# Performance work log

Hardware: AMD Instinct MI355X
Metric: run time of the kernel (lower is better)

## Reference

```python
import jax, jax.numpy as jnp
import numpy as np

LN_EPS = 1e-5
BITS = 4
MAX_VAL = (1 << (BITS - 1)) - 1  # 7 for 4-bit


def fwht(x):
    """Unnormalized fast Walsh-Hadamard transform along the last axis.
    Equivalent to the recursive torch hadamard_transform (H_n = H2 (x) H_{n/2})."""
    orig_shape = x.shape
    n = orig_shape[-1]
    x = x.reshape(-1, n)
    h = 1
    while h < n:
        x = x.reshape(-1, n // (2 * h), 2, h)
        a, b = x[:, :, 0, :], x[:, :, 1, :]
        x = jnp.stack([a + b, a - b], axis=2)
        x = x.reshape(-1, n)
        h *= 2
    return x.reshape(orig_shape)


def layer_norm(x, gamma, beta):
    mu = jnp.mean(x, axis=-1, keepdims=True)
    var = jnp.mean(jnp.square(x - mu), axis=-1, keepdims=True)
    return (x - mu) * jax.lax.rsqrt(var + LN_EPS) * gamma + beta


def activation_quantize(x):
    scale = jnp.clip(jnp.max(jnp.abs(x), axis=-1, keepdims=True), 1e-6, 1e6)
    sf = jnp.clip(MAX_VAL / scale, 1e-6, 1e6)
    return jnp.clip(jnp.round(x * sf), -MAX_VAL, MAX_VAL)


def weight_quantize(w):
    scale = jnp.mean(jnp.abs(w))
    wq = jnp.where(w > 0.5 * scale, 1.0, jnp.where(w < -0.5 * scale, -1.0, 0.0))
    return wq, scale


def setup_inputs() -> dict:
    key = jax.random.key(0)
    k1, k2 = jax.random.split(key)
    B, S, D_IN, D_OUT = 4, 2048, 4096, 4096
    x = jax.random.normal(k1, (B, S, D_IN), dtype=jnp.float32)
    gamma = jnp.ones((D_IN,), dtype=jnp.float32)
    beta = jnp.zeros((D_IN,), dtype=jnp.float32)
    # kaiming_uniform with a=sqrt(5): bound = sqrt(6/((1+5)*fan_in)) = 1/sqrt(fan_in)
    bound = 1.0 / np.sqrt(D_IN)
    weight = jax.random.uniform(k2, (D_OUT, D_IN), dtype=jnp.float32,
                                minval=-bound, maxval=bound)
    return {"x": x, "gamma": gamma, "beta": beta, "weight": weight}


def reference(x, gamma, beta, weight):
    x_ln = layer_norm(x, gamma, beta)            # [B,S,D]
    x_q = activation_quantize(x_ln)              # 4-bit values in [-7,7]
    x_h = fwht(x_q)                              # Hadamard of quantized acts
    w_q, w_scale = weight_quantize(weight)       # ternary * scalar scale
    out = jnp.einsum('bsd,od->bso', x_h, w_q * w_scale)
    out = fwht(out)                              # Hadamard on outputs
    return out
```

## Files before the change

kernel.cpp:

```cpp
#include <hip/hip_runtime.h>
#include <stdint.h>

typedef int i32x4 __attribute__((ext_vector_type(4)));

#define PIDX(e) ((e) + ((e) >> 5))

__device__ __forceinline__ float wred_sum(float v) {
#pragma unroll
    for (int o = 32; o > 0; o >>= 1) v += __shfl_down(v, o, 64);
    return v;
}
__device__ __forceinline__ float wred_max(float v) {
#pragma unroll
    for (int o = 32; o > 0; o >>= 1) v = fmaxf(v, __shfl_down(v, o, 64));
    return v;
}
__device__ __forceinline__ float bred_sum(float v, float* sb, int tid) {
    v = wred_sum(v);
    __syncthreads();
    if ((tid & 63) == 0) sb[tid >> 6] = v;
    __syncthreads();
    return sb[0] + sb[1] + sb[2] + sb[3];
}
__device__ __forceinline__ float bred_max(float v, float* sb, int tid) {
    v = wred_max(v);
    __syncthreads();
    if ((tid & 63) == 0) sb[tid >> 6] = v;
    __syncthreads();
    return fmaxf(fmaxf(sb[0], sb[1]), fmaxf(sb[2], sb[3]));
}

__device__ __forceinline__ int pack4(int a, int b, int c, int d) {
    return (a & 0xff) | ((b & 0xff) << 8) | ((c & 0xff) << 16) | ((d & 0xff) << 24);
}

__device__ __forceinline__ void fwht16(float v[16]) {
#pragma unroll
    for (int h = 1; h < 16; h <<= 1) {
#pragma unroll
        for (int i = 0; i < 16; ++i) {
            if ((i & h) == 0) {
                float a = v[i], b = v[i + h];
                v[i] = a + b;
                v[i + h] = a - b;
            }
        }
    }
}

__device__ void fwht4096(float* f, int t) {
    __syncthreads();
    float v[16];
    {
        int base = t << 4;
#pragma unroll
        for (int i = 0; i < 16; ++i) v[i] = f[PIDX(base + i)];
        fwht16(v);
#pragma unroll
        for (int i = 0; i < 16; ++i) f[PIDX(base + i)] = v[i];
    }
    __syncthreads();
    {
        int base = ((t >> 4) << 8) | (t & 15);
#pragma unroll
        for (int i = 0; i < 16; ++i) v[i] = f[PIDX(base + (i << 4))];
        fwht16(v);
#pragma unroll
        for (int i = 0; i < 16; ++i) f[PIDX(base + (i << 4))] = v[i];
    }
    __syncthreads();
    {
        int base = t;
#pragma unroll
        for (int i = 0; i < 16; ++i) v[i] = f[PIDX(base + (i << 8))];
        fwht16(v);
#pragma unroll
        for (int i = 0; i < 16; ++i) f[PIDX(base + (i << 8))] = v[i];
    }
    __syncthreads();
}

__global__ __launch_bounds__(256) void k_wabs(const float* __restrict__ w,
                                              float* __restrict__ partials) {
    __shared__ float sb[4];
    const int t = threadIdx.x;
    const int b = blockIdx.x;
    float acc = 0.0f;
#pragma unroll
    for (int i = 0; i < 8; ++i) {
        float4 f = *(const float4*)(w + (size_t)(b * 2048 + i * 256 + t) * 4);
        acc += fabsf(f.x) + fabsf(f.y) + fabsf(f.z) + fabsf(f.w);
    }
    float tot = bred_sum(acc, sb, t);
    if (t == 0) partials[b] = tot;
}

__global__ __launch_bounds__(256) void k_wscale(const float* __restrict__ partials,
                                                float* __restrict__ sfinal) {
    __shared__ float sb[4];
    const int t = threadIdx.x;
    float a = 0.0f;
#pragma unroll
    for (int i = 0; i < 8; ++i) a += partials[t + i * 256];
    float tot = bred_sum(a, sb, t);
    if (t == 0) sfinal[0] = tot * (1.0f / 16777216.0f);
}

__global__ __launch_bounds__(256) void k_wprep(const float* __restrict__ w,
                                               const float* __restrict__ sfinal,
                                               int8_t* __restrict__ hi,
                                               int8_t* __restrict__ lo) {
    __shared__ float f[4224];
    const int t = threadIdx.x;
    const int o = blockIdx.x;
    const float thr = 0.5f * sfinal[0];
    const float* wr = w + (size_t)o * 4096;
#pragma unroll
    for (int j = 0; j < 4; ++j) {
        float4 g = *(const float4*)(wr + j * 1024 + t * 4);
        int e = j * 1024 + t * 4;
        f[PIDX(e + 0)] = (g.x > thr) ? 1.0f : ((g.x < -thr) ? -1.0f : 0.0f);
        f[PIDX(e + 1)] = (g.y > thr) ? 1.0f : ((g.y < -thr) ? -1.0f : 0.0f);
        f[PIDX(e + 2)] = (g.z > thr) ? 1.0f : ((g.z < -thr) ? -1.0f : 0.0f);
        f[PIDX(e + 3)] = (g.w > thr) ? 1.0f : ((g.w < -thr) ? -1.0f : 0.0f);
    }
    fwht4096(f, t);
    int* hi32 = (int*)hi;
    int* lo32 = (int*)lo;
#pragma unroll
    for (int j = 0; j < 4; ++j) {
        int e = j * 1024 + t * 4;
        int l4[4], h4[4];
#pragma unroll
        for (int q = 0; q < 4; ++q) {
            int v = __float2int_rn(f[PIDX(e + q)]);
            int lv = ((v + 128) & 255) - 128;
            int hv = (v - lv) >> 8;
            l4[q] = lv; h4[q] = hv;
        }
        lo32[(size_t)o * 1024 + j * 256 + t] = pack4(l4[0], l4[1], l4[2], l4[3]);
        hi32[(size_t)o * 1024 + j * 256 + t] = pack4(h4[0], h4[1], h4[2], h4[3]);
    }
}

__global__ __launch_bounds__(256) void k_lnq(const float* __restrict__ x,
                                             const float* __restrict__ gamma,
                                             const float* __restrict__ beta,
                                             int8_t* __restrict__ xq) {
    __shared__ float sb[4];
    const int t = threadIdx.x;
    const size_t row = blockIdx.x;
    const float* xr = x + row * 4096;
    float v[16];
#pragma unroll
    for (int j = 0; j < 4; ++j) {
        float4 g = *(const float4*)(xr + j * 1024 + t * 4);
        v[j * 4 + 0] = g.x; v[j * 4 + 1] = g.y; v[j * 4 + 2] = g.z; v[j * 4 + 3] = g.w;
    }
    float s = 0.0f;
#pragma unroll
    for (int i = 0; i < 16; ++i) s += v[i];
    const float mu = bred_sum(s, sb, t) * (1.0f / 4096.0f);
    float sq = 0.0f;
#pragma unroll
    for (int i = 0; i < 16; ++i) { float d = v[i] - mu; sq += d * d; }
    const float var = bred_sum(sq, sb, t) * (1.0f / 4096.0f);
    const float rstd = rsqrtf(var + 1e-5f);
#pragma unroll
    for (int j = 0; j < 4; ++j) {
        float4 g = *(const float4*)(gamma + j * 1024 + t * 4);
        float4 b = *(const float4*)(beta + j * 1024 + t * 4);
        v[j * 4 + 0] = (v[j * 4 + 0] - mu) * rstd * g.x + b.x;
        v[j * 4 + 1] = (v[j * 4 + 1] - mu) * rstd * g.y + b.y;
        v[j * 4 + 2] = (v[j * 4 + 2] - mu) * rstd * g.z + b.z;
        v[j * 4 + 3] = (v[j * 4 + 3] - mu) * rstd * g.w + b.w;
    }
    float am = 0.0f;
#pragma unroll
    for (int i = 0; i < 16; ++i) am = fmaxf(am, fabsf(v[i]));
    am = bred_max(am, sb, t);
    const float scale = fminf(fmaxf(am, 1e-6f), 1e6f);
    const float sf = fminf(fmaxf(7.0f / scale, 1e-6f), 1e6f);
    int* xq32 = (int*)xq;
#pragma unroll
    for (int j = 0; j < 4; ++j) {
        int q4[4];
#pragma unroll
        for (int q = 0; q < 4; ++q) {
            float qq = rintf(v[j * 4 + q] * sf);
            qq = fminf(fmaxf(qq, -7.0f), 7.0f);
            q4[q] = (int)qq;
        }
        xq32[row * 1024 + j * 256 + t] = pack4(q4[0], q4[1], q4[2], q4[3]);
    }
}

__device__ __forceinline__ void gl_lds16(const void* g, void* l) {
    __builtin_amdgcn_global_load_lds(
        (const __attribute__((address_space(1))) void*)g,
        (__attribute__((address_space(3))) void*)l, 16, 0, 0);
}

__global__ __launch_bounds__(256, 2) void k_gemm(const int8_t* __restrict__ xq,
                                                 const int8_t* __restrict__ hi,
                                                 const int8_t* __restrict__ lo,
                                                 const float* __restrict__ sfinal,
                                                 float* __restrict__ out) {
    __shared__ __align__(16) int8_t sA[128 * 64];
    __shared__ __align__(16) int8_t sH[128 * 64];
    __shared__ __align__(16) int8_t sL[128 * 64];
    const int tid = threadIdx.x;
    const int lane = tid & 63, wid = tid >> 6;
    const int wr = wid >> 1, wc = wid & 1;
    const int bid = blockIdx.x;
    const int wg = (bid & 7) * 256 + (bid >> 3);
    const int bm = wg & 63, bn = wg >> 6;
    const int row0 = bm * 128, col0 = bn * 128;

    const int srow = lane >> 2;
    const int csw = ((lane & 3) ^ ((srow >> 1) & 3)) * 16;
    const int8_t* gA = xq + (size_t)(row0 + wid * 32 + srow) * 4096 + csw;
    const int8_t* gH = hi + (size_t)(col0 + wid * 32 + srow) * 4096 + csw;
    const int8_t* gL = lo + (size_t)(col0 + wid * 32 + srow) * 4096 + csw;
    int8_t* lA = sA + wid * 2048 + lane * 16;
    int8_t* lH = sH + wid * 2048 + lane * 16;
    int8_t* lL = sL + wid * 2048 + lane * 16;

    const int frow = lane & 15;
    const int pr = ((lane >> 4) ^ ((frow >> 1) & 3)) * 16;
    const int aoff = (wr * 64 + frow) * 64 + pr;
    const int boff = (wc * 64 + frow) * 64 + pr;

    i32x4 accL[4][4] = {};
    i32x4 accH[4][4] = {};

    for (int kt = 0; kt < 4096; kt += 64) {
        gl_lds16(gA + kt, lA);
        gl_lds16(gA + kt + 16 * 4096, lA + 1024);
        gl_lds16(gH + kt, lH);
        gl_lds16(gH + kt + 16 * 4096, lH + 1024);
        gl_lds16(gL + kt, lL);
        gl_lds16(gL + kt + 16 * 4096, lL + 1024);
        __syncthreads();

        i32x4 a[4], bh[4], bl[4];
#pragma unroll
        for (int m = 0; m < 4; ++m) a[m] = *(const i32x4*)(sA + aoff + m * 1024);
#pragma unroll
        for (int n = 0; n < 4; ++n) {
            bh[n] = *(const i32x4*)(sH + boff + n * 1024);
            bl[n] = *(const i32x4*)(sL + boff + n * 1024);
        }
#pragma unroll
        for (int m = 0; m < 4; ++m)
#pragma unroll
            for (int n = 0; n < 4; ++n) {
                accL[m][n] = __builtin_amdgcn_mfma_i32_16x16x64_i8(a[m], bl[n], accL[m][n], 0, 0, 0);
                accH[m][n] = __builtin_amdgcn_mfma_i32_16x16x64_i8(a[m], bh[n], accH[m][n], 0, 0, 0);
            }
        __syncthreads();
    }

    const float s = sfinal[0];
    const int orow0 = row0 + wr * 64 + (lane >> 4) * 4;
    const int ocol0 = col0 + wc * 64 + frow;
#pragma unroll
    for (int m = 0; m < 4; ++m)
#pragma unroll
        for (int n = 0; n < 4; ++n)
#pragma unroll
            for (int r = 0; r < 4; ++r) {
                int val = accL[m][n][r] + (accH[m][n][r] << 8);
                out[(size_t)(orow0 + m * 16 + r) * 4096 + (ocol0 + n * 16)] = s * (float)val;
            }
}

__global__ __launch_bounds__(256) void k_fwht_out(float* __restrict__ out) {
    __shared__ float f[4224];
    const int t = threadIdx.x;
    float* row = out + (size_t)blockIdx.x * 4096;
#pragma unroll
    for (int j = 0; j < 4; ++j) {
        float4 g = *(const float4*)(row + j * 1024 + t * 4);
        int e = j * 1024 + t * 4;
        f[PIDX(e + 0)] = g.x; f[PIDX(e + 1)] = g.y;
        f[PIDX(e + 2)] = g.z; f[PIDX(e + 3)] = g.w;
    }
    fwht4096(f, t);
#pragma unroll
    for (int j = 0; j < 4; ++j) {
        int e = j * 1024 + t * 4;
        float4 g;
        g.x = f[PIDX(e + 0)]; g.y = f[PIDX(e + 1)];
        g.z = f[PIDX(e + 2)]; g.w = f[PIDX(e + 3)];
        *(float4*)(row + e) = g;
    }
}

extern "C" void kernel_launch(void* const* d_in, const int* in_sizes, int n_in,
                              void* d_out, int out_size, void* d_ws, size_t ws_size,
                              hipStream_t stream) {
    const float* x     = (const float*)d_in[0];
    const float* gamma = (const float*)d_in[1];
    const float* beta  = (const float*)d_in[2];
    const float* w     = (const float*)d_in[3];
    float* out = (float*)d_out;

    char* ws = (char*)d_ws;
    float* sfinal   = (float*)ws;
    float* partials = (float*)(ws + 256);
    int8_t* xq  = (int8_t*)(ws + 16384);
    int8_t* whi = (int8_t*)(ws + 16384 + 33554432);
    int8_t* wlo = (int8_t*)(ws + 16384 + 33554432 + 16777216);

    k_wabs  <<<2048, 256, 0, stream>>>(w, partials);
    k_wscale<<<   1, 256, 0, stream>>>(partials, sfinal);
    k_wprep <<<4096, 256, 0, stream>>>(w, sfinal, whi, wlo);
    k_lnq   <<<8192, 256, 0, stream>>>(x, gamma, beta, xq);
    k_gemm  <<<2048, 256, 0, stream>>>(xq, whi, wlo, sfinal, out);
    k_fwht_out<<<8192, 256, 0, stream>>>(out);
}
```

Before: 620.6 us.

## Double-buffer int8 GEMM with 256x128 tiles, 8 waves and split MFMA phases

Result: slower. 725.5 us (+16.9%).

```diff
diff --git a/kernel.cpp b/kernel.cpp
--- a/kernel.cpp
+++ b/kernel.cpp
@@ -201,69 +201,120 @@
         (__attribute__((address_space(3))) void*)l, 16, 0, 0);
 }
 
-__global__ __launch_bounds__(256, 2) void k_gemm(const int8_t* __restrict__ xq,
+__global__ __launch_bounds__(512, 2) void k_gemm(const int8_t* __restrict__ xq,
                                                  const int8_t* __restrict__ hi,
                                                  const int8_t* __restrict__ lo,
                                                  const float* __restrict__ sfinal,
                                                  float* __restrict__ out) {
-    __shared__ __align__(16) int8_t sA[128 * 64];
-    __shared__ __align__(16) int8_t sH[128 * 64];
-    __shared__ __align__(16) int8_t sL[128 * 64];
+    __shared__ __align__(16) int8_t sA[2][16384];
+    __shared__ __align__(16) int8_t sH[2][8192];
+    __shared__ __align__(16) int8_t sL[2][8192];
     const int tid = threadIdx.x;
     const int lane = tid & 63, wid = tid >> 6;
-    const int wr = wid >> 1, wc = wid & 1;
+    const int wm = wid >> 1, wn = wid & 1;
     const int bid = blockIdx.x;
-    const int wg = (bid & 7) * 256 + (bid >> 3);
-    const int bm = wg & 63, bn = wg >> 6;
-    const int row0 = bm * 128, col0 = bn * 128;
-
-    const int srow = lane >> 2;
-    const int csw = ((lane & 3) ^ ((srow >> 1) & 3)) * 16;
-    const int8_t* gA = xq + (size_t)(row0 + wid * 32 + srow) * 4096 + csw;
-    const int8_t* gH = hi + (size_t)(col0 + wid * 32 + srow) * 4096 + csw;
-    const int8_t* gL = lo + (size_t)(col0 + wid * 32 + srow) * 4096 + csw;
-    int8_t* lA = sA + wid * 2048 + lane * 16;
-    int8_t* lH = sH + wid * 2048 + lane * 16;
-    int8_t* lL = sL + wid * 2048 + lane * 16;
+    const int wg = (bid & 7) * 128 + (bid >> 3);
+    const int bm = wg & 31, bn = wg >> 5;
+    const int row0 = bm * 256, col0 = bn * 128;
+
+    const int srow = tid >> 2;
+    const int scol = (((tid & 3) ^ ((srow >> 1) & 3))) * 16;
+    const int8_t* gA0 = xq + (size_t)(row0 + srow) * 4096 + scol;
+    const int8_t* gA1 = gA0 + (size_t)128 * 4096;
+    const int8_t* gH0 = hi + (size_t)(col0 + srow) * 4096 + scol;
+    const int8_t* gL0 = lo + (size_t)(col0 + srow) * 4096 + scol;
+    int8_t* dA = (int8_t*)sA + tid * 16;
+    int8_t* dH = (int8_t*)sH + tid * 16;
+    int8_t* dL = (int8_t*)sL + tid * 16;
+
+#define STAGE(buf_, kt_) do { const int o_ = (kt_) * 64;            \
+        gl_lds16(gA0 + o_, dA + (buf_) * 16384);                    \
+        gl_lds16(gA1 + o_, dA + (buf_) * 16384 + 8192);             \
+        gl_lds16(gH0 + o_, dH + (buf_) * 8192);                     \
+        gl_lds16(gL0 + o_, dL + (buf_) * 8192); } while (0)
 
     const int frow = lane & 15;
-    const int pr = ((lane >> 4) ^ ((frow >> 1) & 3)) * 16;
-    const int aoff = (wr * 64 + frow) * 64 + pr;
-    const int boff = (wc * 64 + frow) * 64 + pr;
+    const int kg = lane >> 4;
+    const int swz = ((kg ^ ((frow >> 1) & 3))) * 16;
+    const int aoff = (wm * 64 + frow) * 64 + swz;
+    const int boff = (wn * 64 + frow) * 64 + swz;
 
     i32x4 accL[4][4] = {};
     i32x4 accH[4][4] = {};
 
-    for (int kt = 0; kt < 4096; kt += 64) {
-        gl_lds16(gA + kt, lA);
-        gl_lds16(gA + kt + 16 * 4096, lA + 1024);
-        gl_lds16(gH + kt, lH);
-        gl_lds16(gH + kt + 16 * 4096, lH + 1024);
-        gl_lds16(gL + kt, lL);
-        gl_lds16(gL + kt + 16 * 4096, lL + 1024);
-        __syncthreads();
-
-        i32x4 a[4], bh[4], bl[4];
-#pragma unroll
-        for (int m = 0; m < 4; ++m) a[m] = *(const i32x4*)(sA + aoff + m * 1024);
-#pragma unroll
-        for (int n = 0; n < 4; ++n) {
-            bh[n] = *(const i32x4*)(sH + boff + n * 1024);
-            bl[n] = *(const i32x4*)(sL + boff + n * 1024);
-        }
-#pragma unroll
-        for (int m = 0; m < 4; ++m)
-#pragma unroll
-            for (int n = 0; n < 4; ++n) {
-                accL[m][n] = __builtin_amdgcn_mfma_i32_16x16x64_i8(a[m], bl[n], accL[m][n], 0, 0, 0);
-                accH[m][n] = __builtin_amdgcn_mfma_i32_16x16x64_i8(a[m], bh[n], accH[m][n], 0, 0, 0);
-            }
-        __syncthreads();
-    }
+    STAGE(0, 0);
+    asm volatile("s_waitcnt vmcnt(0)" ::: "memory");
+    asm volatile("s_barrier" ::: "memory");
+
+    for (int kt = 0; kt < 64; ++kt) {
+        const int cur = kt & 1;
+        const int8_t* A = sA[cur];
+        const int8_t* H = sH[cur];
+        const int8_t* L = sL[cur];
+
+        if (kt < 63) STAGE(cur ^ 1, kt + 1);
+        i32x4 a0 = *(const i32x4*)(A + aoff);
+        i32x4 a1 = *(const i32x4*)(A + aoff + 1024);
+        i32x4 a2 = *(const i32x4*)(A + aoff + 2048);
+        i32x4 a3 = *(const i32x4*)(A + aoff + 3072);
+        i32x4 h0 = *(const i32x4*)(H + boff);
+        i32x4 h1 = *(const i32x4*)(H + boff + 1024);
+        i32x4 l0 = *(const i32x4*)(L + boff);
+        i32x4 l1 = *(const i32x4*)(L + boff + 1024);
+        asm volatile("s_barrier" ::: "memory");
+        asm volatile("s_waitcnt lgkmcnt(0)" ::: "memory");
+        __builtin_amdgcn_s_setprio(1);
+        accL[0][0] = __builtin_amdgcn_mfma_i32_16x16x64_i8(a0, l0, accL[0][0], 0, 0, 0);
+        accH[0][0] = __builtin_amdgcn_mfma_i32_16x16x64_i8(a0, h0, accH[0][0], 0, 0, 0);
+        accL[0][1] = __builtin_amdgcn_mfma_i32_16x16x64_i8(a0, l1, accL[0][1], 0, 0, 0);
+        accH[0][1] = __builtin_amdgcn_mfma_i32_16x16x64_i8(a0, h1, accH[0][1], 0, 0, 0);
+        accL[1][0] = __builtin_amdgcn_mfma_i32_16x16x64_i8(a1, l0, accL[1][0], 0, 0, 0);
+        accH[1][0] = __builtin_amdgcn_mfma_i32_16x16x64_i8(a1, h0, accH[1][0], 0, 0, 0);
+        accL[1][1] = __builtin_amdgcn_mfma_i32_16x16x64_i8(a1, l1, accL[1][1], 0, 0, 0);
+        accH[1][1] = __builtin_amdgcn_mfma_i32_16x16x64_i8(a1, h1, accH[1][1], 0, 0, 0);
+        accL[2][0] = __builtin_amdgcn_mfma_i32_16x16x64_i8(a2, l0, accL[2][0], 0, 0, 0);
+        accH[2][0] = __builtin_amdgcn_mfma_i32_16x16x64_i8(a2, h0, accH[2][0], 0, 0, 0);
+        accL[2][1] = __builtin_amdgcn_mfma_i32_16x16x64_i8(a2, l1, accL[2][1], 0, 0, 0);
+        accH[2][1] = __builtin_amdgcn_mfma_i32_16x16x64_i8(a2, h1, accH[2][1], 0, 0, 0);
+        accL[3][0] = __builtin_amdgcn_mfma_i32_16x16x64_i8(a3, l0, accL[3][0], 0, 0, 0);
+        accH[3][0] = __builtin_amdgcn_mfma_i32_16x16x64_i8(a3, h0, accH[3][0], 0, 0, 0);
+        accL[3][1] = __builtin_amdgcn_mfma_i32_16x16x64_i8(a3, l1, accL[3][1], 0, 0, 0);
+        accH[3][1] = __builtin_amdgcn_mfma_i32_16x16x64_i8(a3, h1, accH[3][1], 0, 0, 0);
+        __builtin_amdgcn_s_setprio(0);
+        asm volatile("s_barrier" ::: "memory");
+
+        i32x4 h2 = *(const i32x4*)(H + boff + 2048);
+        i32x4 h3 = *(const i32x4*)(H + boff + 3072);
+        i32x4 l2 = *(const i32x4*)(L + boff + 2048);
+        i32x4 l3 = *(const i32x4*)(L + boff + 3072);
+        asm volatile("s_barrier" ::: "memory");
+        asm volatile("s_waitcnt lgkmcnt(0)" ::: "memory");
+        __builtin_amdgcn_s_setprio(1);
+        accL[0][2] = __builtin_amdgcn_mfma_i32_16x16x64_i8(a0, l2, accL[0][2], 0, 0, 0);
+        accH[0][2] = __builtin_amdgcn_mfma_i32_16x16x64_i8(a0, h2, accH[0][2], 0, 0, 0);
+        accL[0][3] = __builtin_amdgcn_mfma_i32_16x16x64_i8(a0, l3, accL[0][3], 0, 0, 0);
+        accH[0][3] = __builtin_amdgcn_mfma_i32_16x16x64_i8(a0, h3, accH[0][3], 0, 0, 0);
+        accL[1][2] = __builtin_amdgcn_mfma_i32_16x16x64_i8(a1, l2, accL[1][2], 0, 0, 0);
+        accH[1][2] = __builtin_amdgcn_mfma_i32_16x16x64_i8(a1, h2, accH[1][2], 0, 0, 0);
+        accL[1][3] = __builtin_amdgcn_mfma_i32_16x16x64_i8(a1, l3, accL[1][3], 0, 0, 0);
+        accH[1][3] = __builtin_amdgcn_mfma_i32_16x16x64_i8(a1, h3, accH[1][3], 0, 0, 0);
+        accL[2][2] = __builtin_amdgcn_mfma_i32_16x16x64_i8(a2, l2, accL[2][2], 0, 0, 0);
+        accH[2][2] = __builtin_amdgcn_mfma_i32_16x16x64_i8(a2, h2, accH[2][2], 0, 0, 0);
+        accL[2][3] = __builtin_amdgcn_mfma_i32_16x16x64_i8(a2, l3, accL[2][3], 0, 0, 0);
+        accH[2][3] = __builtin_amdgcn_mfma_i32_16x16x64_i8(a2, h3, accH[2][3], 0, 0, 0);
+        accL[3][2] = __builtin_amdgcn_mfma_i32_16x16x64_i8(a3, l2, accL[3][2], 0, 0, 0);
+        accH[3][2] = __builtin_amdgcn_mfma_i32_16x16x64_i8(a3, h2, accH[3][2], 0, 0, 0);
+        accL[3][3] = __builtin_amdgcn_mfma_i32_16x16x64_i8(a3, l3, accL[3][3], 0, 0, 0);
+        accH[3][3] = __builtin_amdgcn_mfma_i32_16x16x64_i8(a3, h3, accH[3][3], 0, 0, 0);
+        __builtin_amdgcn_s_setprio(0);
+        asm volatile("s_waitcnt vmcnt(0)" ::: "memory");
+        asm volatile("s_barrier" ::: "memory");
+    }
+#undef STAGE
 
     const float s = sfinal[0];
-    const int orow0 = row0 + wr * 64 + (lane >> 4) * 4;
-    const int ocol0 = col0 + wc * 64 + frow;
+    const int orow0 = row0 + wm * 64 + kg * 4;
+    const int ocol0 = col0 + wn * 64 + frow;
 #pragma unroll
     for (int m = 0; m < 4; ++m)
 #pragma unroll
@@ -317,6 +368,6 @@
     k_wscale<<<   1, 256, 0, stream>>>(partials, sfinal);
     k_wprep <<<4096, 256, 0, stream>>>(w, sfinal, whi, wlo);
     k_lnq   <<<8192, 256, 0, stream>>>(x, gamma, beta, xq);
-    k_gemm  <<<2048, 256, 0, stream>>>(xq, whi, wlo, sfinal, out);
+    k_gemm  <<<1024, 512, 0, stream>>>(xq, whi, wlo, sfinal, out);
     k_fwht_out<<<8192, 256, 0, stream>>>(out);
 }
```
